# Kernel tuning notes

Hardware: AMD Instinct MI355X
Metric: run time of the kernel (lower is better)

The kernel has to match this reference:

```python
import jax, jax.numpy as jnp
import numpy as np

ATT_PROP = 2  # config['att_prop']
NEG_BIAS = 1e23


def _bucket(d):
    # standard coref-style distance bucketing into 10 buckets
    d = jnp.abs(d)
    return jnp.where(d <= 4, d,
           jnp.where(d <= 7, 5,
           jnp.where(d <= 15, 6,
           jnp.where(d <= 31, 7,
           jnp.where(d <= 63, 8, 9))))).astype(jnp.int32)


def setup_inputs() -> dict:
    key = jax.random.key(0)
    ks = jax.random.split(key, 12)
    B, N, M, D, H = 2, 1024, 2048, 512, 64
    scale = 0.02  # init_weights_std

    update = jax.random.normal(ks[0], (B, N, D), jnp.float32)
    span_begin = jnp.sort(jax.random.randint(ks[1], (B, N), 0, 2000), axis=-1).astype(jnp.int32)
    span_end = (span_begin + jax.random.randint(ks[2], (B, N), 0, 10)).astype(jnp.int32)
    square_mask = jnp.ones((B, N, N), jnp.float32)
    cand_span_vecs = jax.random.normal(ks[3], (B, M, D), jnp.float32)
    # unique prune indices per batch (a pruned span maps to one candidate slot)
    prune_indices_hoi = jnp.stack([
        jnp.sort(jax.random.permutation(jax.random.fold_in(ks[4], b), M)[:N])
        for b in range(B)]).astype(jnp.int32)
    span_lengths = jnp.array([900, 1024], dtype=jnp.int32)

    W_left = jax.random.normal(ks[5], (D, H), jnp.float32) * scale
    W_right = jax.random.normal(ks[6], (D, H), jnp.float32) * scale
    b_h = jnp.zeros((H,), jnp.float32)
    dist_emb = jax.random.normal(ks[7], (10, H), jnp.float32) * scale
    v_out = jax.random.normal(ks[8], (H,), jnp.float32) * scale
    b_out = jnp.zeros((), jnp.float32)
    W_gate = jax.random.normal(ks[9], (2 * D, D), jnp.float32) * scale
    b_gate = jnp.zeros((D,), jnp.float32)

    return dict(update=update, square_mask=square_mask, cand_span_vecs=cand_span_vecs,
                span_begin=span_begin, span_end=span_end,
                prune_indices_hoi=prune_indices_hoi, span_lengths=span_lengths,
                W_left=W_left, W_right=W_right, b_h=b_h, dist_emb=dist_emb,
                v_out=v_out, b_out=b_out, W_gate=W_gate, b_gate=b_gate)


def reference(update, square_mask, cand_span_vecs, span_begin, span_end,
              prune_indices_hoi, span_lengths, W_left, W_right, b_h,
              dist_emb, v_out, b_out, W_gate, b_gate):
    B, N, D = update.shape
    # pairwise distance features are iteration-invariant: precompute once
    dist = dist_emb[_bucket(span_begin[:, :, None] - span_begin[:, None, :])]  # [B,N,N,H]
    bias = -(1.0 - square_mask) * NEG_BIAS  # [B,N,N]

    for _ in range(ATT_PROP):
        left = update @ W_left    # [B,N,H]
        right = update @ W_right  # [B,N,H]
        h = jax.nn.relu(left[:, :, None, :] + right[:, None, :, :] + dist + b_h)  # [B,N,N,H]
        scores = jnp.einsum('bijh,h->bij', h, v_out) + b_out  # [B,N,N]
        probs = jax.nn.softmax(scores + bias, axis=-1)
        ctxt = jnp.einsum('bij,bjd->bid', probs, update)  # [B,N,D]
        g = jax.nn.sigmoid(jnp.concatenate([update, ctxt], axis=-1) @ W_gate + b_gate)
        update = g * update + (1.0 - g) * ctxt

    # overwrite_spans_hoi: scatter first span_lengths[b] updated vectors back
    valid = jnp.arange(N) < span_lengths[:, None]  # [B,N]

    def scatter_one(cand, idx, upd, m):
        cur = cand[idx]  # [N,D]
        vals = jnp.where(m[:, None], upd, cur)  # invalid rows write back original
        return cand.at[idx].set(vals)

    cand_new = jax.vmap(scatter_one)(cand_span_vecs, prune_indices_hoi, update, valid)
    return cand_new, update
```

## Files before the change

kernel.cpp:

```cpp
#include <hip/hip_runtime.h>
#include <cstdint>

#define NB 2
#define NN 1024
#define MM 2048
#define DD 512
#define HH 64
#define ST 68
#define STB 72

typedef __attribute__((ext_vector_type(8))) short bf16x8;
typedef __attribute__((ext_vector_type(4))) float f32x4;

__device__ inline ushort f2bf(float x) {
  union { float f; uint32_t u; } v; v.f = x;
  uint32_t u = v.u;
  u += 0x7FFF + ((u >> 16) & 1);
  return (ushort)(u >> 16);
}
__device__ inline float bflo(uint32_t d) { return __uint_as_float(d << 16); }
__device__ inline float bfhi(uint32_t d) { return __uint_as_float(d & 0xFFFF0000u); }

#define GLDS(gp, lp) \
  __builtin_amdgcn_global_load_lds( \
      (const __attribute__((address_space(1))) void*)(gp), \
      (__attribute__((address_space(3))) void*)(lp), 16, 0, 0)

__global__ __launch_bounds__(256) void lr_kernel(
    const float* __restrict__ U, const float* __restrict__ Wl,
    const float* __restrict__ Wr, float* __restrict__ left,
    ushort* __restrict__ right_bf) {
  __shared__ float u[8][DD];
  const int block = blockIdx.x;
  const int tid = threadIdx.x;
  const float4* Uv = (const float4*)(U + (size_t)block * 8 * DD);
  float4* uv = (float4*)&u[0][0];
#pragma unroll
  for (int t = 0; t < 4; ++t) uv[tid + t * 256] = Uv[tid + t * 256];
  __syncthreads();
  const int h = tid & 63;
  const int isR = (tid >> 6) & 1;
  const int rbase = tid >> 7;
  const float* __restrict__ W = isR ? Wr : Wl;
  float acc[4] = {0.f, 0.f, 0.f, 0.f};
  for (int k0 = 0; k0 < DD; k0 += 4) {
    float w0 = W[(k0 + 0) * HH + h];
    float w1 = W[(k0 + 1) * HH + h];
    float w2 = W[(k0 + 2) * HH + h];
    float w3 = W[(k0 + 3) * HH + h];
#pragma unroll
    for (int r = 0; r < 4; ++r) {
      float4 u4 = *(const float4*)&u[rbase + r * 2][k0];
      acc[r] = fmaf(u4.w, w3, fmaf(u4.z, w2, fmaf(u4.y, w1, fmaf(u4.x, w0, acc[r]))));
    }
  }
  if (isR) {
#pragma unroll
    for (int r = 0; r < 4; ++r)
      right_bf[(size_t)(block * 8 + rbase + r * 2) * HH + h] = f2bf(acc[r]);
  } else {
#pragma unroll
    for (int r = 0; r < 4; ++r)
      left[(size_t)(block * 8 + rbase + r * 2) * HH + h] = acc[r];
  }
}

__global__ __launch_bounds__(256) void conv_t(
    const float* __restrict__ in, ushort* __restrict__ out_row,
    ushort* __restrict__ out_T, int R, int C, int write_row) {
  __shared__ float tile[64][65];
  const int b = blockIdx.z;
  const int r0 = blockIdx.y * 64, c0 = blockIdx.x * 64;
  const int tx = threadIdx.x & 15, ty = threadIdx.x >> 4;
  const float* inb = in + (size_t)b * R * C;
#pragma unroll
  for (int p = 0; p < 4; ++p) {
    const int r = ty + p * 16;
    const float4 v = *(const float4*)&inb[(size_t)(r0 + r) * C + c0 + tx * 4];
    tile[r][tx * 4 + 0] = v.x; tile[r][tx * 4 + 1] = v.y;
    tile[r][tx * 4 + 2] = v.z; tile[r][tx * 4 + 3] = v.w;
    if (write_row) {
      ushort4 o = make_ushort4(f2bf(v.x), f2bf(v.y), f2bf(v.z), f2bf(v.w));
      *(ushort4*)&out_row[(size_t)b * R * C + (size_t)(r0 + r) * C + c0 + tx * 4] = o;
    }
  }
  __syncthreads();
  ushort* oT = out_T + (size_t)b * R * C;
#pragma unroll
  for (int p = 0; p < 4; ++p) {
    const int rr = ty + p * 16;
    ushort4 o;
    o.x = f2bf(tile[tx * 4 + 0][rr]);
    o.y = f2bf(tile[tx * 4 + 1][rr]);
    o.z = f2bf(tile[tx * 4 + 2][rr]);
    o.w = f2bf(tile[tx * 4 + 3][rr]);
    *(ushort4*)&oT[(size_t)(c0 + rr) * R + r0 + tx * 4] = o;
  }
}

__global__ __launch_bounds__(256) void score_softmax(
    const float* __restrict__ left, const ushort* __restrict__ right_bf,
    const int* __restrict__ span_begin, const float* __restrict__ mask,
    const float* __restrict__ dist_emb, const float* __restrict__ b_h,
    const float* __restrict__ v_out, ushort* __restrict__ probs_bf) {
  __shared__ ushort Rt[64][STB];
  __shared__ ushort LDb[4][10][STB];
  __shared__ float Dbh[10][ST];
  __shared__ float Lt[4][ST];
  __shared__ float Sc[4][NN];
  __shared__ int sbj[NN];
  const int b = blockIdx.y;
  const int r0 = blockIdx.x * 4;
  const int tid = threadIdx.x;
  const int wave = tid >> 6, lane = tid & 63;
  const int row = r0 + wave;

  for (int f = tid; f < 160; f += 256) {
    int bk = f >> 4, h4 = f & 15;
    float4 d = *(const float4*)&dist_emb[bk * HH + h4 * 4];
    float4 bh = *(const float4*)&b_h[h4 * 4];
    d.x += bh.x; d.y += bh.y; d.z += bh.z; d.w += bh.w;
    *(float4*)&Dbh[bk][h4 * 4] = d;
  }
  if (tid < 64) {
    int r = tid >> 4, h4 = tid & 15;
    *(float4*)&Lt[r][h4 * 4] =
        *(const float4*)&left[((size_t)b * NN + r0 + r) * HH + h4 * 4];
  }
  for (int t = tid; t < NN; t += 256) sbj[t] = span_begin[b * NN + t];
  __syncthreads();
  for (int f = tid; f < 2560; f += 256) {
    int i = f >> 9;
    i = f / 640;
    int rem = f - i * 640;
    int bk = rem >> 6, h = rem & 63;
    LDb[i][bk][h] = f2bf(Lt[i][h] + Dbh[bk][h]);
  }
  float4 vr[16];
#pragma unroll
  for (int hq = 0; hq < 16; ++hq) vr[hq] = *(const float4*)&v_out[hq * 4];
  const int my_sbi = span_begin[(size_t)b * NN + row];
  const float* maskrow = mask + ((size_t)b * NN + row) * NN;

#pragma unroll 1
  for (int c = 0; c < 16; ++c) {
    __syncthreads();
#pragma unroll
    for (int t = 0; t < 2; ++t) {
      const int f = tid + t * 256;
      const int r = f >> 3, u8 = f & 7;
      *(bf16x8*)&Rt[r][u8 * 8] =
          *(const bf16x8*)&right_bf[((size_t)b * NN + c * 64 + r) * HH + u8 * 8];
    }
    __syncthreads();
    int d = sbj[c * 64 + lane] - my_sbi;
    d = d < 0 ? -d : d;
    const int bk =
        d <= 4 ? d : (d <= 7 ? 5 : (d <= 15 ? 6 : (d <= 31 ? 7 : (d <= 63 ? 8 : 9))));
    const ushort* zp = &LDb[wave][bk][0];
    const ushort* rp = &Rt[lane][0];
    float acc = 0.f;
#pragma unroll
    for (int oct = 0; oct < 8; ++oct) {
      const uint4 zd = *(const uint4*)&zp[oct * 8];
      const uint4 rd = *(const uint4*)&rp[oct * 8];
      const float4 v0 = vr[2 * oct], v1 = vr[2 * oct + 1];
      acc = fmaf(fmaxf(bflo(zd.x) + bflo(rd.x), 0.f), v0.x, acc);
      acc = fmaf(fmaxf(bfhi(zd.x) + bfhi(rd.x), 0.f), v0.y, acc);
      acc = fmaf(fmaxf(bflo(zd.y) + bflo(rd.y), 0.f), v0.z, acc);
      acc = fmaf(fmaxf(bfhi(zd.y) + bfhi(rd.y), 0.f), v0.w, acc);
      acc = fmaf(fmaxf(bflo(zd.z) + bflo(rd.z), 0.f), v1.x, acc);
      acc = fmaf(fmaxf(bfhi(zd.z) + bfhi(rd.z), 0.f), v1.y, acc);
      acc = fmaf(fmaxf(bflo(zd.w) + bflo(rd.w), 0.f), v1.z, acc);
      acc = fmaf(fmaxf(bfhi(zd.w) + bfhi(rd.w), 0.f), v1.w, acc);
    }
    const float mval = maskrow[c * 64 + lane];
    Sc[wave][c * 64 + lane] = acc - (1.0f - mval) * 1e23f;
  }
  float mx = -3.0e38f;
#pragma unroll
  for (int c = 0; c < 16; ++c) mx = fmaxf(mx, Sc[wave][c * 64 + lane]);
#pragma unroll
  for (int off = 32; off; off >>= 1) mx = fmaxf(mx, __shfl_xor(mx, off));
  float sum = 0.f;
#pragma unroll
  for (int c = 0; c < 16; ++c) {
    const float e = __expf(Sc[wave][c * 64 + lane] - mx);
    Sc[wave][c * 64 + lane] = e;
    sum += e;
  }
#pragma unroll
  for (int off = 32; off; off >>= 1) sum += __shfl_xor(sum, off);
  const float inv = 1.0f / sum;
  ushort* prow = probs_bf + ((size_t)b * NN + row) * NN;
#pragma unroll
  for (int c = 0; c < 16; ++c)
    prow[c * 64 + lane] = f2bf(Sc[wave][c * 64 + lane] * inv);
}

__global__ __launch_bounds__(256) void gemm_ctxt_mfma(
    const ushort* __restrict__ Pbf, const ushort* __restrict__ UT,
    ushort* __restrict__ Cbf) {
  __shared__ ushort As[64 * 64];
  __shared__ ushort Bs[64 * 64];
  const int b = blockIdx.z;
  const int m0 = blockIdx.y * 64, n0 = blockIdx.x * 64;
  const int tid = threadIdx.x;
  const int lane = tid & 63, wave = tid >> 6;
  const int wm = (wave >> 1) * 32, wn = (wave & 1) * 32;
  const ushort* Ab = Pbf + (size_t)b * NN * NN;
  const ushort* Bb = UT + (size_t)b * DD * NN;
  f32x4 acc[2][2] = {};
  const int fm = lane & 15, quad = lane >> 4;
  for (int k0 = 0; k0 < NN; k0 += 64) {
#pragma unroll
    for (int t = 0; t < 2; ++t) {
      const int idx = tid + t * 256;
      const int r = idx >> 3, c8 = idx & 7;
      const int g = c8 ^ (r & 7);
      GLDS(Ab + (size_t)(m0 + r) * NN + k0 + g * 8, As + idx * 8);
      GLDS(Bb + (size_t)(n0 + r) * NN + k0 + g * 8, Bs + idx * 8);
    }
    __syncthreads();
#pragma unroll
    for (int s = 0; s < 2; ++s) {
      bf16x8 af[2], bfr[2];
#pragma unroll
      for (int tm = 0; tm < 2; ++tm) {
        const int row = wm + tm * 16 + fm;
        const int c8 = (s * 4 + quad) ^ (row & 7);
        af[tm] = *(const bf16x8*)&As[row * 64 + c8 * 8];
      }
#pragma unroll
      for (int tn = 0; tn < 2; ++tn) {
        const int row = wn + tn * 16 + fm;
        const int c8 = (s * 4 + quad) ^ (row & 7);
        bfr[tn] = *(const bf16x8*)&Bs[row * 64 + c8 * 8];
      }
#pragma unroll
      for (int tm = 0; tm < 2; ++tm)
#pragma unroll
        for (int tn = 0; tn < 2; ++tn)
          acc[tm][tn] = __builtin_amdgcn_mfma_f32_16x16x32_bf16(
              af[tm], bfr[tn], acc[tm][tn], 0, 0, 0);
    }
    __syncthreads();
  }
#pragma unroll
  for (int tm = 0; tm < 2; ++tm)
#pragma unroll
    for (int tn = 0; tn < 2; ++tn) {
      const int col = n0 + wn + tn * 16 + fm;
#pragma unroll
      for (int r = 0; r < 4; ++r) {
        const int row = m0 + wm + tm * 16 + quad * 4 + r;
        Cbf[(size_t)b * NN * DD + (size_t)row * DD + col] = f2bf(acc[tm][tn][r]);
      }
    }
}

__global__ __launch_bounds__(256) void gemm_gate_mfma(
    const ushort* __restrict__ Ubf, const ushort* __restrict__ Cbf,
    const ushort* __restrict__ WgT, const float* __restrict__ bg,
    const float* __restrict__ Uf, float* __restrict__ Uout,
    ushort* __restrict__ UbfOut, ushort* __restrict__ UTOut) {
  __shared__ ushort As[64 * 64];
  __shared__ ushort Bs[64 * 64];
  __shared__ ushort Tt[64][66];
  const int b = blockIdx.z;
  const int m0 = blockIdx.y * 64, n0 = blockIdx.x * 64;
  const int tid = threadIdx.x;
  const int lane = tid & 63, wave = tid >> 6;
  const int wm = (wave >> 1) * 32, wn = (wave & 1) * 32;
  f32x4 acc[2][2] = {};
  const int fm = lane & 15, quad = lane >> 4;
  for (int k0 = 0; k0 < 2 * DD; k0 += 64) {
    const ushort* Abase = (k0 < DD) ? (Ubf + (size_t)b * NN * DD)
                                    : (Cbf + (size_t)b * NN * DD);
    const int kc = k0 & (DD - 1);
#pragma unroll
    for (int t = 0; t < 2; ++t) {
      const int idx = tid + t * 256;
      const int r = idx >> 3, c8 = idx & 7;
      const int g = c8 ^ (r & 7);
      GLDS(Abase + (size_t)(m0 + r) * DD + kc + g * 8, As + idx * 8);
      GLDS(WgT + (size_t)(n0 + r) * (2 * DD) + k0 + g * 8, Bs + idx * 8);
    }
    __syncthreads();
#pragma unroll
    for (int s = 0; s < 2; ++s) {
      bf16x8 af[2], bfr[2];
#pragma unroll
      for (int tm = 0; tm < 2; ++tm) {
        const int row = wm + tm * 16 + fm;
        const int c8 = (s * 4 + quad) ^ (row & 7);
        af[tm] = *(const bf16x8*)&As[row * 64 + c8 * 8];
      }
#pragma unroll
      for (int tn = 0; tn < 2; ++tn) {
        const int row = wn + tn * 16 + fm;
        const int c8 = (s * 4 + quad) ^ (row & 7);
        bfr[tn] = *(const bf16x8*)&Bs[row * 64 + c8 * 8];
      }
#pragma unroll
      for (int tm = 0; tm < 2; ++tm)
#pragma unroll
        for (int tn = 0; tn < 2; ++tn)
          acc[tm][tn] = __builtin_amdgcn_mfma_f32_16x16x32_bf16(
              af[tm], bfr[tn], acc[tm][tn], 0, 0, 0);
    }
    __syncthreads();
  }
#pragma unroll
  for (int tm = 0; tm < 2; ++tm)
#pragma unroll
    for (int tn = 0; tn < 2; ++tn) {
      const int cl = wn + tn * 16 + fm;
      const int col = n0 + cl;
      const float bgv = bg[col];
#pragma unroll
      for (int r = 0; r < 4; ++r) {
        const int rl = wm + tm * 16 + quad * 4 + r;
        const int row = m0 + rl;
        const size_t off = (size_t)b * NN * DD + (size_t)row * DD + col;
        const float g = 1.f / (1.f + __expf(-(acc[tm][tn][r] + bgv)));
        const float cv = __uint_as_float(((uint32_t)Cbf[off]) << 16);
        const float o = g * Uf[off] + (1.f - g) * cv;
        Uout[off] = o;
        const ushort ob = f2bf(o);
        UbfOut[off] = ob;
        Tt[rl][cl] = ob;
      }
    }
  __syncthreads();
#pragma unroll
  for (int p = 0; p < 4; ++p) {
    const int cl = (tid >> 4) + p * 16;
    const int rl = (tid & 15) * 4;
    ushort4 o;
    o.x = Tt[rl + 0][cl]; o.y = Tt[rl + 1][cl];
    o.z = Tt[rl + 2][cl]; o.w = Tt[rl + 3][cl];
    *(ushort4*)&UTOut[((size_t)b * DD + n0 + cl) * NN + m0 + rl] = o;
  }
}

__global__ __launch_bounds__(256) void out_copy(
    const float* __restrict__ cand, const float* __restrict__ upd,
    float* __restrict__ out) {
  const int t = blockIdx.x * 256 + threadIdx.x;
  float4* o4 = (float4*)out;
  if (t < 524288) o4[t] = ((const float4*)cand)[t];
  else o4[t] = ((const float4*)upd)[t - 524288];
}

__global__ __launch_bounds__(128) void scatter_k(
    float* __restrict__ out_cand, const float* __restrict__ upd,
    const int* __restrict__ prune, const int* __restrict__ span_len) {
  const int row = blockIdx.x;
  const int b = row >> 10, i = row & 1023;
  if (i >= span_len[b]) return;
  const int dst = prune[row];
  const float4* src = (const float4*)(upd + (size_t)row * DD);
  float4* d = (float4*)(out_cand + ((size_t)b * MM + dst) * DD);
  d[threadIdx.x] = src[threadIdx.x];
}

extern "C" void kernel_launch(void* const* d_in, const int* in_sizes, int n_in,
                              void* d_out, int out_size, void* d_ws, size_t ws_size,
                              hipStream_t stream) {
  const float* update = (const float*)d_in[0];
  const float* mask = (const float*)d_in[1];
  const float* cand = (const float*)d_in[2];
  const int* span_begin = (const int*)d_in[3];
  const int* prune = (const int*)d_in[5];
  const int* span_len = (const int*)d_in[6];
  const float* Wl = (const float*)d_in[7];
  const float* Wr = (const float*)d_in[8];
  const float* b_h = (const float*)d_in[9];
  const float* dist_emb = (const float*)d_in[10];
  const float* v_out = (const float*)d_in[11];
  const float* Wg = (const float*)d_in[13];
  const float* b_gate = (const float*)d_in[14];

  char* w = (char*)d_ws;
  float* left = (float*)w;        w += (size_t)NB * NN * HH * 4;
  ushort* right_bf = (ushort*)w;  w += (size_t)NB * NN * HH * 2;
  ushort* probs_bf = (ushort*)w;  w += (size_t)NB * NN * NN * 2;
  ushort* ctxt_bf = (ushort*)w;   w += (size_t)NB * NN * DD * 2;
  float* upd1 = (float*)w;        w += (size_t)NB * NN * DD * 4;
  float* upd2 = (float*)w;        w += (size_t)NB * NN * DD * 4;
  ushort* Ubf0 = (ushort*)w;      w += (size_t)NB * NN * DD * 2;
  ushort* Ubf1 = (ushort*)w;      w += (size_t)NB * NN * DD * 2;
  ushort* UT = (ushort*)w;        w += (size_t)NB * NN * DD * 2;
  ushort* WgT = (ushort*)w;       w += (size_t)2 * DD * DD * 2;

  float* out = (float*)d_out;

  conv_t<<<dim3(8, 16, 1), 256, 0, stream>>>(Wg, WgT, WgT, 2 * DD, DD, 0);
  conv_t<<<dim3(8, 16, NB), 256, 0, stream>>>(update, Ubf0, UT, NN, DD, 1);

  const float* Ucur = update;
  float* nexts[2] = {upd1, upd2};
  ushort* ubf_in[2] = {Ubf0, Ubf1};
  ushort* ubf_out[2] = {Ubf1, Ubf0};
  for (int it = 0; it < 2; ++it) {
    lr_kernel<<<256, 256, 0, stream>>>(Ucur, Wl, Wr, left, right_bf);
    score_softmax<<<dim3(NN / 4, NB), 256, 0, stream>>>(
        left, right_bf, span_begin, mask, dist_emb, b_h, v_out, probs_bf);
    gemm_ctxt_mfma<<<dim3(8, 16, NB), 256, 0, stream>>>(probs_bf, UT, ctxt_bf);
    gemm_gate_mfma<<<dim3(8, 16, NB), 256, 0, stream>>>(
        ubf_in[it], ctxt_bf, WgT, b_gate, Ucur, nexts[it], ubf_out[it], UT);
    Ucur = nexts[it];
  }
  out_copy<<<3072, 256, 0, stream>>>(cand, Ucur, out);
  scatter_k<<<NB * NN, 128, 0, stream>>>(out, Ucur, prune, span_len);
}
```

Baseline: 240.1 us.

## Fuse prep kernels, fold final copy/scatter into gate GEMM, halve lr rows per block

Merges the two transpose/convert launches, the first left/right projection, and the candidate copy into one prep kernel. The final gate GEMM now writes the updated vectors straight to the output and scatters them into the candidate rows, which removes the separate out_copy and scatter kernels. lr_kernel handles 4 rows per block across 512 blocks for more parallelism, and the score loop uses two accumulators for more ILP. Together these cut launch count and intermediate memory traffic. The cost is a heavier prep kernel and a scatter inside the GEMM epilogue that relies on candidate rows being written only after the copy finishes, which holds because the launches are stream-ordered.

```diff
diff --git a/kernel.cpp b/kernel.cpp
--- a/kernel.cpp
+++ b/kernel.cpp
@@ -26,75 +26,137 @@
       (const __attribute__((address_space(1))) void*)(gp), \
       (__attribute__((address_space(3))) void*)(lp), 16, 0, 0)
 
+__global__ __launch_bounds__(256) void prep_kernel(
+    const float* __restrict__ Wg, ushort* __restrict__ WgT,
+    const float* __restrict__ update, ushort* __restrict__ Ubf0,
+    ushort* __restrict__ UT, const float* __restrict__ cand,
+    float* __restrict__ out, const float* __restrict__ Wl,
+    const float* __restrict__ Wr, float* __restrict__ left,
+    ushort* __restrict__ right_bf) {
+  __shared__ __align__(16) char smem[16640];
+  const int bid = blockIdx.x;
+  const int tid = threadIdx.x;
+  const int tx = tid & 15, ty = tid >> 4;
+
+  if (bid < 384) {
+    const float* in;
+    ushort* out_row;
+    ushort* out_T;
+    int R, C, r0, c0;
+    if (bid < 128) {
+      in = Wg; out_row = nullptr; out_T = WgT;
+      R = 2 * DD; C = DD; r0 = (bid >> 3) * 64; c0 = (bid & 7) * 64;
+    } else {
+      const int t = bid - 128, b = t >> 7, rem = t & 127;
+      in = update + (size_t)b * NN * DD;
+      out_row = Ubf0 + (size_t)b * NN * DD;
+      out_T = UT + (size_t)b * DD * NN;
+      R = NN; C = DD; r0 = (rem >> 3) * 64; c0 = (rem & 7) * 64;
+    }
+    float (*tile)[65] = (float(*)[65])smem;
+#pragma unroll
+    for (int p = 0; p < 4; ++p) {
+      const int r = ty + p * 16;
+      const float4 v = *(const float4*)&in[(size_t)(r0 + r) * C + c0 + tx * 4];
+      tile[r][tx * 4 + 0] = v.x; tile[r][tx * 4 + 1] = v.y;
+      tile[r][tx * 4 + 2] = v.z; tile[r][tx * 4 + 3] = v.w;
+      if (out_row) {
+        ushort4 o = make_ushort4(f2bf(v.x), f2bf(v.y), f2bf(v.z), f2bf(v.w));
+        *(ushort4*)&out_row[(size_t)(r0 + r) * C + c0 + tx * 4] = o;
+      }
+    }
+    __syncthreads();
+#pragma unroll
+    for (int p = 0; p < 4; ++p) {
+      const int rr = ty + p * 16;
+      ushort4 o;
+      o.x = f2bf(tile[tx * 4 + 0][rr]);
+      o.y = f2bf(tile[tx * 4 + 1][rr]);
+      o.z = f2bf(tile[tx * 4 + 2][rr]);
+      o.w = f2bf(tile[tx * 4 + 3][rr]);
+      *(ushort4*)&out_T[(size_t)(c0 + rr) * R + r0 + tx * 4] = o;
+    }
+    __syncthreads();
+  }
+
+  {
+    float (*u)[DD] = (float(*)[DD])smem;
+    const float4* Uv = (const float4*)(update + (size_t)bid * 4 * DD);
+    float4* uv = (float4*)&u[0][0];
+#pragma unroll
+    for (int t = 0; t < 2; ++t) uv[tid + t * 256] = Uv[tid + t * 256];
+    __syncthreads();
+    const int h = tid & 63;
+    const int isR = (tid >> 6) & 1;
+    const int rsel = tid >> 7;
+    const float* __restrict__ W = isR ? Wr : Wl;
+    float acc[2] = {0.f, 0.f};
+    for (int k0 = 0; k0 < DD; k0 += 4) {
+      float w0 = W[(k0 + 0) * HH + h];
+      float w1 = W[(k0 + 1) * HH + h];
+      float w2 = W[(k0 + 2) * HH + h];
+      float w3 = W[(k0 + 3) * HH + h];
+#pragma unroll
+      for (int r = 0; r < 2; ++r) {
+        float4 u4 = *(const float4*)&u[rsel + r * 2][k0];
+        acc[r] = fmaf(u4.w, w3, fmaf(u4.z, w2, fmaf(u4.y, w1, fmaf(u4.x, w0, acc[r]))));
+      }
+    }
+    if (isR) {
+#pragma unroll
+      for (int r = 0; r < 2; ++r)
+        right_bf[(size_t)(bid * 4 + rsel + r * 2) * HH + h] = f2bf(acc[r]);
+    } else {
+#pragma unroll
+      for (int r = 0; r < 2; ++r)
+        left[(size_t)(bid * 4 + rsel + r * 2) * HH + h] = acc[r];
+    }
+  }
+
+  {
+    const float4* c4 = (const float4*)cand;
+    float4* o4 = (float4*)out;
+    for (int idx = bid * 256 + tid; idx < NB * MM * DD / 4; idx += 512 * 256)
+      o4[idx] = c4[idx];
+  }
+}
+
 __global__ __launch_bounds__(256) void lr_kernel(
     const float* __restrict__ U, const float* __restrict__ Wl,
     const float* __restrict__ Wr, float* __restrict__ left,
     ushort* __restrict__ right_bf) {
-  __shared__ float u[8][DD];
-  const int block = blockIdx.x;
+  __shared__ float u[4][DD];
+  const int bid = blockIdx.x;
   const int tid = threadIdx.x;
-  const float4* Uv = (const float4*)(U + (size_t)block * 8 * DD);
+  const float4* Uv = (const float4*)(U + (size_t)bid * 4 * DD);
   float4* uv = (float4*)&u[0][0];
 #pragma unroll
-  for (int t = 0; t < 4; ++t) uv[tid + t * 256] = Uv[tid + t * 256];
+  for (int t = 0; t < 2; ++t) uv[tid + t * 256] = Uv[tid + t * 256];
   __syncthreads();
   const int h = tid & 63;
   const int isR = (tid >> 6) & 1;
-  const int rbase = tid >> 7;
+  const int rsel = tid >> 7;
   const float* __restrict__ W = isR ? Wr : Wl;
-  float acc[4] = {0.f, 0.f, 0.f, 0.f};
+  float acc[2] = {0.f, 0.f};
   for (int k0 = 0; k0 < DD; k0 += 4) {
     float w0 = W[(k0 + 0) * HH + h];
     float w1 = W[(k0 + 1) * HH + h];
     float w2 = W[(k0 + 2) * HH + h];
     float w3 = W[(k0 + 3) * HH + h];
 #pragma unroll
-    for (int r = 0; r < 4; ++r) {
-      float4 u4 = *(const float4*)&u[rbase + r * 2][k0];
+    for (int r = 0; r < 2; ++r) {
+      float4 u4 = *(const float4*)&u[rsel + r * 2][k0];
       acc[r] = fmaf(u4.w, w3, fmaf(u4.z, w2, fmaf(u4.y, w1, fmaf(u4.x, w0, acc[r]))));
     }
   }
   if (isR) {
 #pragma unroll
-    for (int r = 0; r < 4; ++r)
-      right_bf[(size_t)(block * 8 + rbase + r * 2) * HH + h] = f2bf(acc[r]);
+    for (int r = 0; r < 2; ++r)
+      right_bf[(size_t)(bid * 4 + rsel + r * 2) * HH + h] = f2bf(acc[r]);
   } else {
 #pragma unroll
-    for (int r = 0; r < 4; ++r)
-      left[(size_t)(block * 8 + rbase + r * 2) * HH + h] = acc[r];
-  }
-}
-
-__global__ __launch_bounds__(256) void conv_t(
-    const float* __restrict__ in, ushort* __restrict__ out_row,
-    ushort* __restrict__ out_T, int R, int C, int write_row) {
-  __shared__ float tile[64][65];
-  const int b = blockIdx.z;
-  const int r0 = blockIdx.y * 64, c0 = blockIdx.x * 64;
-  const int tx = threadIdx.x & 15, ty = threadIdx.x >> 4;
-  const float* inb = in + (size_t)b * R * C;
-#pragma unroll
-  for (int p = 0; p < 4; ++p) {
-    const int r = ty + p * 16;
-    const float4 v = *(const float4*)&inb[(size_t)(r0 + r) * C + c0 + tx * 4];
-    tile[r][tx * 4 + 0] = v.x; tile[r][tx * 4 + 1] = v.y;
-    tile[r][tx * 4 + 2] = v.z; tile[r][tx * 4 + 3] = v.w;
-    if (write_row) {
-      ushort4 o = make_ushort4(f2bf(v.x), f2bf(v.y), f2bf(v.z), f2bf(v.w));
-      *(ushort4*)&out_row[(size_t)b * R * C + (size_t)(r0 + r) * C + c0 + tx * 4] = o;
-    }
-  }
-  __syncthreads();
-  ushort* oT = out_T + (size_t)b * R * C;
-#pragma unroll
-  for (int p = 0; p < 4; ++p) {
-    const int rr = ty + p * 16;
-    ushort4 o;
-    o.x = f2bf(tile[tx * 4 + 0][rr]);
-    o.y = f2bf(tile[tx * 4 + 1][rr]);
-    o.z = f2bf(tile[tx * 4 + 2][rr]);
-    o.w = f2bf(tile[tx * 4 + 3][rr]);
-    *(ushort4*)&oT[(size_t)(c0 + rr) * R + r0 + tx * 4] = o;
+    for (int r = 0; r < 2; ++r)
+      left[(size_t)(bid * 4 + rsel + r * 2) * HH + h] = acc[r];
   }
 }
 
@@ -130,8 +192,7 @@
   for (int t = tid; t < NN; t += 256) sbj[t] = span_begin[b * NN + t];
   __syncthreads();
   for (int f = tid; f < 2560; f += 256) {
-    int i = f >> 9;
-    i = f / 640;
+    int i = f / 640;
     int rem = f - i * 640;
     int bk = rem >> 6, h = rem & 63;
     LDb[i][bk][h] = f2bf(Lt[i][h] + Dbh[bk][h]);
@@ -159,23 +220,38 @@
         d <= 4 ? d : (d <= 7 ? 5 : (d <= 15 ? 6 : (d <= 31 ? 7 : (d <= 63 ? 8 : 9))));
     const ushort* zp = &LDb[wave][bk][0];
     const ushort* rp = &Rt[lane][0];
-    float acc = 0.f;
-#pragma unroll
-    for (int oct = 0; oct < 8; ++oct) {
-      const uint4 zd = *(const uint4*)&zp[oct * 8];
-      const uint4 rd = *(const uint4*)&rp[oct * 8];
-      const float4 v0 = vr[2 * oct], v1 = vr[2 * oct + 1];
-      acc = fmaf(fmaxf(bflo(zd.x) + bflo(rd.x), 0.f), v0.x, acc);
-      acc = fmaf(fmaxf(bfhi(zd.x) + bfhi(rd.x), 0.f), v0.y, acc);
-      acc = fmaf(fmaxf(bflo(zd.y) + bflo(rd.y), 0.f), v0.z, acc);
-      acc = fmaf(fmaxf(bfhi(zd.y) + bfhi(rd.y), 0.f), v0.w, acc);
-      acc = fmaf(fmaxf(bflo(zd.z) + bflo(rd.z), 0.f), v1.x, acc);
-      acc = fmaf(fmaxf(bfhi(zd.z) + bfhi(rd.z), 0.f), v1.y, acc);
-      acc = fmaf(fmaxf(bflo(zd.w) + bflo(rd.w), 0.f), v1.z, acc);
-      acc = fmaf(fmaxf(bfhi(zd.w) + bfhi(rd.w), 0.f), v1.w, acc);
+    float acc0 = 0.f, acc1 = 0.f;
+#pragma unroll
+    for (int oct = 0; oct < 8; oct += 2) {
+      {
+        const uint4 zd = *(const uint4*)&zp[oct * 8];
+        const uint4 rd = *(const uint4*)&rp[oct * 8];
+        const float4 v0 = vr[2 * oct], v1 = vr[2 * oct + 1];
+        acc0 = fmaf(fmaxf(bflo(zd.x) + bflo(rd.x), 0.f), v0.x, acc0);
+        acc0 = fmaf(fmaxf(bfhi(zd.x) + bfhi(rd.x), 0.f), v0.y, acc0);
+        acc0 = fmaf(fmaxf(bflo(zd.y) + bflo(rd.y), 0.f), v0.z, acc0);
+        acc0 = fmaf(fmaxf(bfhi(zd.y) + bfhi(rd.y), 0.f), v0.w, acc0);
+        acc0 = fmaf(fmaxf(bflo(zd.z) + bflo(rd.z), 0.f), v1.x, acc0);
+        acc0 = fmaf(fmaxf(bfhi(zd.z) + bfhi(rd.z), 0.f), v1.y, acc0);
+        acc0 = fmaf(fmaxf(bflo(zd.w) + bflo(rd.w), 0.f), v1.z, acc0);
+        acc0 = fmaf(fmaxf(bfhi(zd.w) + bfhi(rd.w), 0.f), v1.w, acc0);
+      }
+      {
+        const uint4 zd = *(const uint4*)&zp[(oct + 1) * 8];
+        const uint4 rd = *(const uint4*)&rp[(oct + 1) * 8];
+        const float4 v0 = vr[2 * oct + 2], v1 = vr[2 * oct + 3];
+        acc1 = fmaf(fmaxf(bflo(zd.x) + bflo(rd.x), 0.f), v0.x, acc1);
+        acc1 = fmaf(fmaxf(bfhi(zd.x) + bfhi(rd.x), 0.f), v0.y, acc1);
+        acc1 = fmaf(fmaxf(bflo(zd.y) + bflo(rd.y), 0.f), v0.z, acc1);
+        acc1 = fmaf(fmaxf(bfhi(zd.y) + bfhi(rd.y), 0.f), v0.w, acc1);
+        acc1 = fmaf(fmaxf(bflo(zd.z) + bflo(rd.z), 0.f), v1.x, acc1);
+        acc1 = fmaf(fmaxf(bfhi(zd.z) + bfhi(rd.z), 0.f), v1.y, acc1);
+        acc1 = fmaf(fmaxf(bflo(zd.w) + bflo(rd.w), 0.f), v1.z, acc1);
+        acc1 = fmaf(fmaxf(bfhi(zd.w) + bfhi(rd.w), 0.f), v1.w, acc1);
+      }
     }
     const float mval = maskrow[c * 64 + lane];
-    Sc[wave][c * 64 + lane] = acc - (1.0f - mval) * 1e23f;
+    Sc[wave][c * 64 + lane] = (acc0 + acc1) - (1.0f - mval) * 1e23f;
   }
   float mx = -3.0e38f;
 #pragma unroll
@@ -263,7 +339,9 @@
     const ushort* __restrict__ Ubf, const ushort* __restrict__ Cbf,
     const ushort* __restrict__ WgT, const float* __restrict__ bg,
     const float* __restrict__ Uf, float* __restrict__ Uout,
-    ushort* __restrict__ UbfOut, ushort* __restrict__ UTOut) {
+    ushort* __restrict__ UbfOut, ushort* __restrict__ UTOut,
+    const int* __restrict__ prune, const int* __restrict__ span_len,
+    float* __restrict__ out_cand, int final_it) {
   __shared__ ushort As[64 * 64];
   __shared__ ushort Bs[64 * 64];
   __shared__ ushort Tt[64][66];
@@ -311,6 +389,7 @@
     }
     __syncthreads();
   }
+  const int slen = span_len[b];
 #pragma unroll
   for (int tm = 0; tm < 2; ++tm)
 #pragma unroll
@@ -327,42 +406,30 @@
         const float cv = __uint_as_float(((uint32_t)Cbf[off]) << 16);
         const float o = g * Uf[off] + (1.f - g) * cv;
         Uout[off] = o;
-        const ushort ob = f2bf(o);
-        UbfOut[off] = ob;
-        Tt[rl][cl] = ob;
-      }
-    }
-  __syncthreads();
-#pragma unroll
-  for (int p = 0; p < 4; ++p) {
-    const int cl = (tid >> 4) + p * 16;
-    const int rl = (tid & 15) * 4;
-    ushort4 o;
-    o.x = Tt[rl + 0][cl]; o.y = Tt[rl + 1][cl];
-    o.z = Tt[rl + 2][cl]; o.w = Tt[rl + 3][cl];
-    *(ushort4*)&UTOut[((size_t)b * DD + n0 + cl) * NN + m0 + rl] = o;
-  }
-}
-
-__global__ __launch_bounds__(256) void out_copy(
-    const float* __restrict__ cand, const float* __restrict__ upd,
-    float* __restrict__ out) {
-  const int t = blockIdx.x * 256 + threadIdx.x;
-  float4* o4 = (float4*)out;
-  if (t < 524288) o4[t] = ((const float4*)cand)[t];
-  else o4[t] = ((const float4*)upd)[t - 524288];
-}
-
-__global__ __launch_bounds__(128) void scatter_k(
-    float* __restrict__ out_cand, const float* __restrict__ upd,
-    const int* __restrict__ prune, const int* __restrict__ span_len) {
-  const int row = blockIdx.x;
-  const int b = row >> 10, i = row & 1023;
-  if (i >= span_len[b]) return;
-  const int dst = prune[row];
-  const float4* src = (const float4*)(upd + (size_t)row * DD);
-  float4* d = (float4*)(out_cand + ((size_t)b * MM + dst) * DD);
-  d[threadIdx.x] = src[threadIdx.x];
+        if (final_it) {
+          if (row < slen) {
+            const int dst = prune[b * NN + row];
+            out_cand[((size_t)b * MM + dst) * DD + col] = o;
+          }
+        } else {
+          const ushort ob = f2bf(o);
+          UbfOut[off] = ob;
+          Tt[rl][cl] = ob;
+        }
+      }
+    }
+  if (!final_it) {
+    __syncthreads();
+#pragma unroll
+    for (int p = 0; p < 4; ++p) {
+      const int cl = (tid >> 4) + p * 16;
+      const int rl = (tid & 15) * 4;
+      ushort4 o;
+      o.x = Tt[rl + 0][cl]; o.y = Tt[rl + 1][cl];
+      o.z = Tt[rl + 2][cl]; o.w = Tt[rl + 3][cl];
+      *(ushort4*)&UTOut[((size_t)b * DD + n0 + cl) * NN + m0 + rl] = o;
+    }
+  }
 }
 
 extern "C" void kernel_launch(void* const* d_in, const int* in_sizes, int n_in,
@@ -388,30 +455,27 @@
   ushort* probs_bf = (ushort*)w;  w += (size_t)NB * NN * NN * 2;
   ushort* ctxt_bf = (ushort*)w;   w += (size_t)NB * NN * DD * 2;
   float* upd1 = (float*)w;        w += (size_t)NB * NN * DD * 4;
-  float* upd2 = (float*)w;        w += (size_t)NB * NN * DD * 4;
   ushort* Ubf0 = (ushort*)w;      w += (size_t)NB * NN * DD * 2;
   ushort* Ubf1 = (ushort*)w;      w += (size_t)NB * NN * DD * 2;
   ushort* UT = (ushort*)w;        w += (size_t)NB * NN * DD * 2;
   ushort* WgT = (ushort*)w;       w += (size_t)2 * DD * DD * 2;
 
   float* out = (float*)d_out;
-
-  conv_t<<<dim3(8, 16, 1), 256, 0, stream>>>(Wg, WgT, WgT, 2 * DD, DD, 0);
-  conv_t<<<dim3(8, 16, NB), 256, 0, stream>>>(update, Ubf0, UT, NN, DD, 1);
-
-  const float* Ucur = update;
-  float* nexts[2] = {upd1, upd2};
-  ushort* ubf_in[2] = {Ubf0, Ubf1};
-  ushort* ubf_out[2] = {Ubf1, Ubf0};
-  for (int it = 0; it < 2; ++it) {
-    lr_kernel<<<256, 256, 0, stream>>>(Ucur, Wl, Wr, left, right_bf);
-    score_softmax<<<dim3(NN / 4, NB), 256, 0, stream>>>(
-        left, right_bf, span_begin, mask, dist_emb, b_h, v_out, probs_bf);
-    gemm_ctxt_mfma<<<dim3(8, 16, NB), 256, 0, stream>>>(probs_bf, UT, ctxt_bf);
-    gemm_gate_mfma<<<dim3(8, 16, NB), 256, 0, stream>>>(
-        ubf_in[it], ctxt_bf, WgT, b_gate, Ucur, nexts[it], ubf_out[it], UT);
-    Ucur = nexts[it];
-  }
-  out_copy<<<3072, 256, 0, stream>>>(cand, Ucur, out);
-  scatter_k<<<NB * NN, 128, 0, stream>>>(out, Ucur, prune, span_len);
-}
+  float* out_upd = out + (size_t)NB * MM * DD;
+
+  prep_kernel<<<512, 256, 0, stream>>>(Wg, WgT, update, Ubf0, UT, cand, out,
+                                       Wl, Wr, left, right_bf);
+  score_softmax<<<dim3(NN / 4, NB), 256, 0, stream>>>(
+      left, right_bf, span_begin, mask, dist_emb, b_h, v_out, probs_bf);
+  gemm_ctxt_mfma<<<dim3(8, 16, NB), 256, 0, stream>>>(probs_bf, UT, ctxt_bf);
+  gemm_gate_mfma<<<dim3(8, 16, NB), 256, 0, stream>>>(
+      Ubf0, ctxt_bf, WgT, b_gate, update, upd1, Ubf1, UT,
+      prune, span_len, out, 0);
+  lr_kernel<<<512, 256, 0, stream>>>(upd1, Wl, Wr, left, right_bf);
+  score_softmax<<<dim3(NN / 4, NB), 256, 0, stream>>>(
+      left, right_bf, span_begin, mask, dist_emb, b_h, v_out, probs_bf);
+  gemm_ctxt_mfma<<<dim3(8, 16, NB), 256, 0, stream>>>(probs_bf, UT, ctxt_bf);
+  gemm_gate_mfma<<<dim3(8, 16, NB), 256, 0, stream>>>(
+      Ubf1, ctxt_bf, WgT, b_gate, upd1, out_upd, nullptr, nullptr,
+      prune, span_len, out, 1);
+}
```

After: 241.2 us. No clear change (+0.5%).
